# Optimization experiments

Measured on AMD Instinct MI355X. Metric: run time of the kernel, lower is better.

## Reference

```python
import jax, jax.numpy as jnp
import numpy as np

T, B, D, H, O = 512, 64, 512, 1024, 512

def _xavier(key, shape):
    fan_out, fan_in = shape
    limit = np.sqrt(6.0 / (fan_in + fan_out))
    return jax.random.uniform(key, shape, jnp.float32, -limit, limit)

def setup_inputs() -> dict:
    key = jax.random.key(0)
    ks = jax.random.split(key, 10)
    x = jax.random.normal(ks[0], (T, B, D), jnp.float32)
    # Gate order: i, f, o, c (stacked along first axis for a fused 4H projection;
    # math identical to 8 separate Linears in the torch module, biases init to 0
    # but we randomize them slightly for a non-trivial reference).
    Wx = jnp.concatenate([_xavier(ks[1 + g], (H, D)) for g in range(4)], axis=0)  # [4H, D]
    Wh = jnp.concatenate([_xavier(ks[5 + g], (H, H)) for g in range(4)], axis=0)  # [4H, H]
    bx = jnp.zeros((4 * H,), jnp.float32)
    bh = jnp.zeros((4 * H,), jnp.float32)
    Why = _xavier(ks[9], (O, H))
    bhy = jnp.zeros((O,), jnp.float32)
    return {"x": x, "Wx": Wx, "bx": bx, "Wh": Wh, "bh": bh, "Why": Why, "bhy": bhy}

def reference(x, Wx, bx, Wh, bh, Why, bhy):
    Hd = Wh.shape[1]
    Bd = x.shape[1]
    # Precompute all input-path projections in one batched GEMM: [T, B, 4H]
    xp = jnp.einsum('tbd,gd->tbg', x, Wx) + bx + bh

    def step(carry, xp_t):
        h, c = carry
        gates = xp_t + h @ Wh.T  # [B, 4H]
        i_t = jax.nn.sigmoid(gates[:, 0 * Hd:1 * Hd])
        f_t = jax.nn.sigmoid(gates[:, 1 * Hd:2 * Hd])
        o_t = jax.nn.sigmoid(gates[:, 2 * Hd:3 * Hd])
        c_tilde = jnp.tanh(gates[:, 3 * Hd:4 * Hd])
        c = f_t * c + i_t * c_tilde
        h = o_t * jnp.tanh(c)
        return (h, c), None

    h0 = jnp.zeros((Bd, Hd), x.dtype)
    c0 = jnp.zeros((Bd, Hd), x.dtype)
    (h, c), _ = jax.lax.scan(step, (h0, c0), xp)
    return h @ Why.T + bhy  # [B, O]
```

## Files before the change

kernel.cpp:

```cpp
#include <hip/hip_runtime.h>
#include <hip/hip_bf16.h>
#include <math.h>

constexpr int T = 512;
constexpr int B = 64;
constexpr int D = 512;
constexpr int H = 1024;
constexpr int O = 512;
constexpr int GROUPS = 2;
constexpr int BG   = B / GROUPS;
constexpr int GBLK = 128;
constexpr int COLS = 32;
constexpr int KCH  = (D + H) / 8;

typedef __attribute__((ext_vector_type(8))) __bf16 bf16x8;
typedef __attribute__((ext_vector_type(4))) float  floatx4;

struct GBar {
    unsigned arr[GBLK][32];
    unsigned gflag[8][32];
};

__global__ __launch_bounds__(256) void convert_w(
    const float* __restrict__ Wx, const float* __restrict__ Wh,
    __bf16* __restrict__ Wc)
{
    const int id = blockIdx.x * 256 + threadIdx.x;
    if (id >= GBLK * KCH * COLS) return;
    const int nl     = id & 31;
    const int kchunk = (id >> 5) % KCH;
    const int strip  = id / (KCH * COLS);
    const int n = strip * COLS + nl;
    const int j = n >> 2, g = n & 3;
    const int k0 = kchunk * 8;
    const float* src = (k0 < D) ? &Wx[(size_t)(g * H + j) * D + k0]
                                : &Wh[(size_t)(g * H + j) * H + (k0 - D)];
    const float4 a = *(const float4*)src;
    const float4 b = *(const float4*)(src + 4);
    __bf16 t8[8] = {(__bf16)a.x,(__bf16)a.y,(__bf16)a.z,(__bf16)a.w,
                    (__bf16)b.x,(__bf16)b.y,(__bf16)b.z,(__bf16)b.w};
    *(uint4*)&Wc[(size_t)id * 8] = *(uint4*)t8;
}

__global__ __launch_bounds__(256) void make_bias(
    const float* __restrict__ bx, const float* __restrict__ bh,
    float* __restrict__ bias)
{
    const int n = blockIdx.x * 256 + threadIdx.x;
    if (n < 4 * H) {
        const int j = n >> 2, g = n & 3;
        bias[n] = bx[g * H + j] + bh[g * H + j];
    }
}

__global__ __launch_bounds__(128, 1) void lstm_persistent(
    const float* __restrict__ x,
    const __bf16* __restrict__ Wc,
    const float* __restrict__ bias,
    __bf16* __restrict__ hbufs,
    float* __restrict__ hfin,
    GBar* bars)
{
    __shared__ __attribute__((aligned(16))) __bf16 wlds[KCH * COLS * 8];

    const int tid   = threadIdx.x;
    const int wid   = tid >> 6;
    const int lane  = tid & 63;
    const int cm    = lane & 15;
    const int q     = lane >> 4;
    const int group = blockIdx.x >> 7;
    const int gb    = blockIdx.x & 127;
    const int n0    = gb * COLS;
    GBar* bar = bars + group;
    __bf16* hb0 = hbufs + (size_t)group * 2 * BG * H;
    __bf16* hb1 = hb0 + BG * H;

    {
        const uint4* wsrc = (const uint4*)(Wc + (size_t)gb * KCH * COLS * 8);
        uint4* wdst = (uint4*)wlds;
        for (int i = tid; i < KCH * COLS; i += 128) wdst[i] = wsrc[i];
    }
    const int p4 = cm & 3;
    const int jl = cm >> 2;
    const int row_l = wid * 16 + q * 4 + p4;
    const float4 bias0q = *(const float4*)&bias[n0 + jl * 4];
    const float4 bias1q = *(const float4*)&bias[n0 + 16 + jl * 4];
    float c0 = 0.f, c1 = 0.f;
    __syncthreads();

    const int grow = group * BG + wid * 16 + cm;
    const float* xrow = x + (size_t)grow * D + q * 8;
    const int    hoff = (wid * 16 + cm) * H + q * 8;
    const __bf16* wl  = wlds + (q * 32 + cm) * 8;

    floatx4 acc[2][2];
    float4  xcur[16][2];

    auto loadx = [&](int tt) {
        const float* xr = xrow + (size_t)tt * (B * D);
        #pragma unroll
        for (int s = 0; s < 16; ++s) {
            xcur[s][0] = *(const float4*)(xr + s * 32);
            xcur[s][1] = *(const float4*)(xr + s * 32 + 4);
        }
    };
    auto xmfma = [&]() {
        acc[0][0] = (floatx4){0,0,0,0}; acc[0][1] = (floatx4){0,0,0,0};
        acc[1][0] = (floatx4){0,0,0,0}; acc[1][1] = (floatx4){0,0,0,0};
        #pragma unroll
        for (int s = 0; s < 16; ++s) {
            const float4 a0 = xcur[s][0], a1 = xcur[s][1];
            const bf16x8 af = {(__bf16)a0.x,(__bf16)a0.y,(__bf16)a0.z,(__bf16)a0.w,
                               (__bf16)a1.x,(__bf16)a1.y,(__bf16)a1.z,(__bf16)a1.w};
            const bf16x8 b0 = *(const bf16x8*)(wl + s * 1024);
            const bf16x8 b1 = *(const bf16x8*)(wl + s * 1024 + 128);
            acc[0][s & 1] = __builtin_amdgcn_mfma_f32_16x16x32_bf16(af, b0, acc[0][s & 1], 0, 0, 0);
            acc[1][s & 1] = __builtin_amdgcn_mfma_f32_16x16x32_bf16(af, b1, acc[1][s & 1], 0, 0, 0);
        }
    };

    auto quadT = [&](float v[4]) {
        float w0 = __shfl_xor(v[1], 1), w1 = __shfl_xor(v[0], 1);
        float w2 = __shfl_xor(v[3], 1), w3 = __shfl_xor(v[2], 1);
        if (p4 & 1) { v[0] = w0; v[2] = w2; } else { v[1] = w1; v[3] = w3; }
        w0 = __shfl_xor(v[2], 2); w1 = __shfl_xor(v[3], 2);
        w2 = __shfl_xor(v[0], 2); w3 = __shfl_xor(v[1], 2);
        if (p4 & 2) { v[0] = w0; v[1] = w1; } else { v[2] = w2; v[3] = w3; }
    };

    loadx(0);
    xmfma();

    const int sub = gb >> 4;

    for (int t = 0; t < T; ++t) {
        const __bf16* hcur = (t & 1) ? hb1 : hb0;
        __bf16*       hnxt = (t & 1) ? hb0 : hb1;

        if (t > 0) {
            while (__hip_atomic_load(&bar->gflag[sub][0], __ATOMIC_RELAXED,
                                     __HIP_MEMORY_SCOPE_AGENT) < (unsigned)t)
                __builtin_amdgcn_s_sleep(1);
        }

        {
            const __bf16* hbase = hcur + hoff;
            uint4 hv[32];
            asm volatile(
                "global_load_dwordx4 %0, %32, off sc0 sc1\n\t"
                "global_load_dwordx4 %1, %32, off offset:64 sc0 sc1\n\t"
                "global_load_dwordx4 %2, %32, off offset:128 sc0 sc1\n\t"
                "global_load_dwordx4 %3, %32, off offset:192 sc0 sc1\n\t"
                "global_load_dwordx4 %4, %32, off offset:256 sc0 sc1\n\t"
                "global_load_dwordx4 %5, %32, off offset:320 sc0 sc1\n\t"
                "global_load_dwordx4 %6, %32, off offset:384 sc0 sc1\n\t"
                "global_load_dwordx4 %7, %32, off offset:448 sc0 sc1\n\t"
                "global_load_dwordx4 %8, %32, off offset:512 sc0 sc1\n\t"
                "global_load_dwordx4 %9, %32, off offset:576 sc0 sc1\n\t"
                "global_load_dwordx4 %10, %32, off offset:640 sc0 sc1\n\t"
                "global_load_dwordx4 %11, %32, off offset:704 sc0 sc1\n\t"
                "global_load_dwordx4 %12, %32, off offset:768 sc0 sc1\n\t"
                "global_load_dwordx4 %13, %32, off offset:832 sc0 sc1\n\t"
                "global_load_dwordx4 %14, %32, off offset:896 sc0 sc1\n\t"
                "global_load_dwordx4 %15, %32, off offset:960 sc0 sc1\n\t"
                "global_load_dwordx4 %16, %32, off offset:1024 sc0 sc1\n\t"
                "global_load_dwordx4 %17, %32, off offset:1088 sc0 sc1\n\t"
                "global_load_dwordx4 %18, %32, off offset:1152 sc0 sc1\n\t"
                "global_load_dwordx4 %19, %32, off offset:1216 sc0 sc1\n\t"
                "global_load_dwordx4 %20, %32, off offset:1280 sc0 sc1\n\t"
                "global_load_dwordx4 %21, %32, off offset:1344 sc0 sc1\n\t"
                "global_load_dwordx4 %22, %32, off offset:1408 sc0 sc1\n\t"
                "global_load_dwordx4 %23, %32, off offset:1472 sc0 sc1\n\t"
                "global_load_dwordx4 %24, %32, off offset:1536 sc0 sc1\n\t"
                "global_load_dwordx4 %25, %32, off offset:1600 sc0 sc1\n\t"
                "global_load_dwordx4 %26, %32, off offset:1664 sc0 sc1\n\t"
                "global_load_dwordx4 %27, %32, off offset:1728 sc0 sc1\n\t"
                "global_load_dwordx4 %28, %32, off offset:1792 sc0 sc1\n\t"
                "global_load_dwordx4 %29, %32, off offset:1856 sc0 sc1\n\t"
                "global_load_dwordx4 %30, %32, off offset:1920 sc0 sc1\n\t"
                "global_load_dwordx4 %31, %32, off offset:1984 sc0 sc1\n\t"
                "s_waitcnt vmcnt(0)"
                : "=&v"(hv[0]),  "=&v"(hv[1]),  "=&v"(hv[2]),  "=&v"(hv[3]),
                  "=&v"(hv[4]),  "=&v"(hv[5]),  "=&v"(hv[6]),  "=&v"(hv[7]),
                  "=&v"(hv[8]),  "=&v"(hv[9]),  "=&v"(hv[10]), "=&v"(hv[11]),
                  "=&v"(hv[12]), "=&v"(hv[13]), "=&v"(hv[14]), "=&v"(hv[15]),
                  "=&v"(hv[16]), "=&v"(hv[17]), "=&v"(hv[18]), "=&v"(hv[19]),
                  "=&v"(hv[20]), "=&v"(hv[21]), "=&v"(hv[22]), "=&v"(hv[23]),
                  "=&v"(hv[24]), "=&v"(hv[25]), "=&v"(hv[26]), "=&v"(hv[27]),
                  "=&v"(hv[28]), "=&v"(hv[29]), "=&v"(hv[30]), "=&v"(hv[31])
                : "v"(hbase)
                : "memory");
            #pragma unroll
            for (int sg = 0; sg < 32; ++sg) {
                union { uint4 u; bf16x8 v; } hf; hf.u = hv[sg];
                const bf16x8 b0 = *(const bf16x8*)(wl + 16384 + sg * 1024);
                const bf16x8 b1 = *(const bf16x8*)(wl + 16384 + sg * 1024 + 128);
                acc[0][sg & 1] = __builtin_amdgcn_mfma_f32_16x16x32_bf16(hf.v, b0, acc[0][sg & 1], 0, 0, 0);
                acc[1][sg & 1] = __builtin_amdgcn_mfma_f32_16x16x32_bf16(hf.v, b1, acc[1][sg & 1], 0, 0, 0);
            }
        }
        const floatx4 av0 = acc[0][0] + acc[0][1];
        const floatx4 av1 = acc[1][0] + acc[1][1];

        float g0v[4] = {av0.x, av0.y, av0.z, av0.w};
        float g1v[4] = {av1.x, av1.y, av1.z, av1.w};
        quadT(g0v);
        quadT(g1v);

        if (t + 1 < T) loadx(t + 1);

        const float i0 = 1.f / (1.f + expf(-(g0v[0] + bias0q.x)));
        const float f0 = 1.f / (1.f + expf(-(g0v[1] + bias0q.y)));
        const float o0 = 1.f / (1.f + expf(-(g0v[2] + bias0q.z)));
        const float t0 = tanhf(g0v[3] + bias0q.w);
        const float i1 = 1.f / (1.f + expf(-(g1v[0] + bias1q.x)));
        const float f1 = 1.f / (1.f + expf(-(g1v[1] + bias1q.y)));
        const float o1 = 1.f / (1.f + expf(-(g1v[2] + bias1q.z)));
        const float t1 = tanhf(g1v[3] + bias1q.w);
        c0 = f0 * c0 + i0 * t0;
        c1 = f1 * c1 + i1 * t1;
        const float hv0 = o0 * tanhf(c0);
        const float hv1 = o1 * tanhf(c1);
        const int j0 = gb * 8 + jl;
        const int hi = row_l * H + j0;
        union { __bf16 b; unsigned short u; } s0, s1;
        s0.b = (__bf16)hv0; s1.b = (__bf16)hv1;
        __hip_atomic_store((unsigned short*)&hnxt[hi], s0.u, __ATOMIC_RELAXED,
                           __HIP_MEMORY_SCOPE_AGENT);
        __hip_atomic_store((unsigned short*)&hnxt[hi + 4], s1.u, __ATOMIC_RELAXED,
                           __HIP_MEMORY_SCOPE_AGENT);
        if (t == T - 1) {
            const int gr = group * BG + row_l;
            hfin[gr * H + j0]     = hv0;
            hfin[gr * H + j0 + 4] = hv1;
        }

        __syncthreads();

        if (tid == 0)
            __hip_atomic_store(&bar->arr[gb][0], (unsigned)(t + 1),
                               __ATOMIC_RELAXED, __HIP_MEMORY_SCOPE_AGENT);

        if (t + 1 < T) xmfma();

        if (gb == 0 && tid < 64) {
            const unsigned want = (unsigned)(t + 1);
            for (;;) {
                const unsigned a = __hip_atomic_load(&bar->arr[2 * tid][0],
                                        __ATOMIC_RELAXED, __HIP_MEMORY_SCOPE_AGENT);
                const unsigned b = __hip_atomic_load(&bar->arr[2 * tid + 1][0],
                                        __ATOMIC_RELAXED, __HIP_MEMORY_SCOPE_AGENT);
                if (__ballot((a >= want) && (b >= want)) == ~0ull) break;
            }
            if (tid < 8)
                __hip_atomic_store(&bar->gflag[tid][0], want,
                                   __ATOMIC_RELAXED, __HIP_MEMORY_SCOPE_AGENT);
        }
    }
}

__global__ __launch_bounds__(256) void out_gemm(
    const float* __restrict__ h, const float* __restrict__ Why,
    const float* __restrict__ bhy, float* __restrict__ out)
{
    const int idx = blockIdx.x * 256 + threadIdx.x;
    if (idx >= B * O) return;
    const int b = idx / O;
    const int o = idx % O;
    const float4* hv = (const float4*)&h[(size_t)b * H];
    const float4* wv = (const float4*)&Why[(size_t)o * H];
    float s = 0.f;
    #pragma unroll 4
    for (int k = 0; k < H / 4; ++k) {
        const float4 a = hv[k];
        const float4 w = wv[k];
        s += a.x * w.x + a.y * w.y + a.z * w.z + a.w * w.w;
    }
    out[idx] = s + bhy[o];
}

extern "C" void kernel_launch(void* const* d_in, const int* in_sizes, int n_in,
                              void* d_out, int out_size, void* d_ws, size_t ws_size,
                              hipStream_t stream) {
    const float* x   = (const float*)d_in[0];
    const float* Wx  = (const float*)d_in[1];
    const float* bx  = (const float*)d_in[2];
    const float* Wh  = (const float*)d_in[3];
    const float* bh  = (const float*)d_in[4];
    const float* Why = (const float*)d_in[5];
    const float* bhy = (const float*)d_in[6];
    float* out = (float*)d_out;

    char* ws = (char*)d_ws;
    __bf16* Wc    = (__bf16*)ws;
    float*  bias  = (float*)(ws + 12582912);
    __bf16* hbufs = (__bf16*)(ws + 12599296);
    GBar*   bars  = (GBar*)  (ws + 12861440);
    float*  hfin  = (float*)ws;

    (void)hipMemsetAsync(ws + 12599296, 0, 262144 + 2 * sizeof(GBar), stream);
    convert_w<<<3072, 256, 0, stream>>>(Wx, Wh, Wc);
    make_bias<<<16, 256, 0, stream>>>(bx, bh, bias);

    lstm_persistent<<<GROUPS * GBLK, 128, 0, stream>>>(x, Wc, bias, hbufs,
                                                       hfin, bars);

    out_gemm<<<(B * O + 255) / 256, 256, 0, stream>>>(hfin, Why, bhy, out);
}
```

Measured before the change: 3.473 ms.

## Replace centralized barrier flag with per-block polling and pack hidden-state stores

The two-hop grid barrier, where block 0 gathered all 128 arrival counters and then broadcast a group flag, is removed. Each block's first wave now polls all 128 arrival counters itself with a ballot and then synchronizes the block, which cuts one cross-block hop from the per-timestep critical path. The weight and bias column permutation is changed so each lane owns two adjacent hidden units, so the two bf16 h values are written as one 32-bit atomic store. In exchange, all blocks poll the shared counters at once, which raises L2 and atomic traffic.

```diff
diff --git a/kernel.cpp b/kernel.cpp
--- a/kernel.cpp
+++ b/kernel.cpp
@@ -18,7 +18,6 @@
 
 struct GBar {
     unsigned arr[GBLK][32];
-    unsigned gflag[8][32];
 };
 
 __global__ __launch_bounds__(256) void convert_w(
@@ -30,8 +29,10 @@
     const int nl     = id & 31;
     const int kchunk = (id >> 5) % KCH;
     const int strip  = id / (KCH * COLS);
-    const int n = strip * COLS + nl;
-    const int j = n >> 2, g = n & 3;
+    const int s  = nl >> 4;
+    const int jl = (nl >> 2) & 3;
+    const int g  = nl & 3;
+    const int j  = strip * 8 + 2 * jl + s;
     const int k0 = kchunk * 8;
     const float* src = (k0 < D) ? &Wx[(size_t)(g * H + j) * D + k0]
                                 : &Wh[(size_t)(g * H + j) * H + (k0 - D)];
@@ -48,7 +49,11 @@
 {
     const int n = blockIdx.x * 256 + threadIdx.x;
     if (n < 4 * H) {
-        const int j = n >> 2, g = n & 3;
+        const int gbn = n >> 5, nl = n & 31;
+        const int s  = nl >> 4;
+        const int jl = (nl >> 2) & 3;
+        const int g  = nl & 3;
+        const int j  = gbn * 8 + 2 * jl + s;
         bias[n] = bx[g * H + j] + bh[g * H + j];
     }
 }
@@ -131,16 +136,23 @@
     loadx(0);
     xmfma();
 
-    const int sub = gb >> 4;
-
     for (int t = 0; t < T; ++t) {
         const __bf16* hcur = (t & 1) ? hb1 : hb0;
         __bf16*       hnxt = (t & 1) ? hb0 : hb1;
 
         if (t > 0) {
-            while (__hip_atomic_load(&bar->gflag[sub][0], __ATOMIC_RELAXED,
-                                     __HIP_MEMORY_SCOPE_AGENT) < (unsigned)t)
-                __builtin_amdgcn_s_sleep(1);
+            if (wid == 0) {
+                const unsigned want = (unsigned)t;
+                for (;;) {
+                    const unsigned a = __hip_atomic_load(&bar->arr[2 * lane][0],
+                                            __ATOMIC_RELAXED, __HIP_MEMORY_SCOPE_AGENT);
+                    const unsigned b = __hip_atomic_load(&bar->arr[2 * lane + 1][0],
+                                            __ATOMIC_RELAXED, __HIP_MEMORY_SCOPE_AGENT);
+                    if (__ballot((a >= want) && (b >= want)) == ~0ull) break;
+                    __builtin_amdgcn_s_sleep(1);
+                }
+            }
+            __syncthreads();
         }
 
         {
@@ -221,18 +233,16 @@
         c1 = f1 * c1 + i1 * t1;
         const float hv0 = o0 * tanhf(c0);
         const float hv1 = o1 * tanhf(c1);
-        const int j0 = gb * 8 + jl;
+        const int j0 = gb * 8 + 2 * jl;
         const int hi = row_l * H + j0;
-        union { __bf16 b; unsigned short u; } s0, s1;
-        s0.b = (__bf16)hv0; s1.b = (__bf16)hv1;
-        __hip_atomic_store((unsigned short*)&hnxt[hi], s0.u, __ATOMIC_RELAXED,
-                           __HIP_MEMORY_SCOPE_AGENT);
-        __hip_atomic_store((unsigned short*)&hnxt[hi + 4], s1.u, __ATOMIC_RELAXED,
+        union { __bf16 h2[2]; unsigned u; } hp;
+        hp.h2[0] = (__bf16)hv0; hp.h2[1] = (__bf16)hv1;
+        __hip_atomic_store((unsigned*)&hnxt[hi], hp.u, __ATOMIC_RELAXED,
                            __HIP_MEMORY_SCOPE_AGENT);
         if (t == T - 1) {
             const int gr = group * BG + row_l;
             hfin[gr * H + j0]     = hv0;
-            hfin[gr * H + j0 + 4] = hv1;
+            hfin[gr * H + j0 + 1] = hv1;
         }
 
         __syncthreads();
@@ -242,20 +252,6 @@
                                __ATOMIC_RELAXED, __HIP_MEMORY_SCOPE_AGENT);
 
         if (t + 1 < T) xmfma();
-
-        if (gb == 0 && tid < 64) {
-            const unsigned want = (unsigned)(t + 1);
-            for (;;) {
-                const unsigned a = __hip_atomic_load(&bar->arr[2 * tid][0],
-                                        __ATOMIC_RELAXED, __HIP_MEMORY_SCOPE_AGENT);
-                const unsigned b = __hip_atomic_load(&bar->arr[2 * tid + 1][0],
-                                        __ATOMIC_RELAXED, __HIP_MEMORY_SCOPE_AGENT);
-                if (__ballot((a >= want) && (b >= want)) == ~0ull) break;
-            }
-            if (tid < 8)
-                __hip_atomic_store(&bar->gflag[tid][0], want,
-                                   __ATOMIC_RELAXED, __HIP_MEMORY_SCOPE_AGENT);
-        }
     }
 }
 
```

Measured after the change: 3.255 ms. 1.07x faster.
